# Kernel optimization log

Measured on AMD Instinct MI355X. Metric: run time of the kernel, lower is better.

## Reference

```python
import jax, jax.numpy as jnp
import numpy as np

EPS = 1e-5

def _gn(x, w, b):
    # GroupNorm with 1 group on [N, C]: normalize each row over C, then affine.
    mu = jnp.mean(x, axis=-1, keepdims=True)
    var = jnp.mean((x - mu) ** 2, axis=-1, keepdims=True)
    return (x - mu) * jax.lax.rsqrt(var + EPS) * w + b

def setup_inputs() -> dict:
    key = jax.random.key(0)
    ks = jax.random.split(key, 24)
    N_AGT, N_CTX, E, D, NC = 50000, 100000, 500000, 128, 2
    s = 0.05  # weight init scale
    inp = {
        "agts": jax.random.normal(ks[0], (N_AGT, D), jnp.float32),
        "ctx": jax.random.normal(ks[1], (N_CTX, D), jnp.float32),
        "agt_ctrs": jax.random.normal(ks[2], (N_AGT, NC), jnp.float32),
        "ctx_ctrs": jax.random.normal(ks[3], (N_CTX, NC), jnp.float32),
        "hi": jax.random.randint(ks[4], (E,), 0, N_AGT, jnp.int32),
        "wi": jax.random.randint(ks[5], (E,), 0, N_CTX, jnp.int32),
        # dist MLP: Linear(2->128, bias) + ReLU, then Linear(128->128 no bias)+GN+ReLU
        "Wd1": jax.random.normal(ks[6], (D, NC), jnp.float32) * s,
        "bd1": jnp.zeros((D,), jnp.float32),
        "Wd2": jax.random.normal(ks[7], (D, D), jnp.float32) * s,
        "gd2w": jnp.ones((D,), jnp.float32), "gd2b": jnp.zeros((D,), jnp.float32),
        # query: Linear(128->128 no bias)+GN+ReLU
        "Wq": jax.random.normal(ks[8], (D, D), jnp.float32) * s,
        "gqw": jnp.ones((D,), jnp.float32), "gqb": jnp.zeros((D,), jnp.float32),
        # ctx MLP: Linear(384->128 no bias)+GN+ReLU, then Linear(128->128 no bias)
        "Wc1": jax.random.normal(ks[9], (D, 3 * D), jnp.float32) * s,
        "gc1w": jnp.ones((D,), jnp.float32), "gc1b": jnp.zeros((D,), jnp.float32),
        "Wc2": jax.random.normal(ks[10], (D, D), jnp.float32) * s,
        # agt linear (no bias), post-scatter GN, final Linear(no bias)+GN
        "Wa": jax.random.normal(ks[11], (D, D), jnp.float32) * s,
        "gnw": jnp.ones((D,), jnp.float32), "gnb": jnp.zeros((D,), jnp.float32),
        "Wl": jax.random.normal(ks[12], (D, D), jnp.float32) * s,
        "glw": jnp.ones((D,), jnp.float32), "glb": jnp.zeros((D,), jnp.float32),
    }
    return inp

def reference(agts, ctx, agt_ctrs, ctx_ctrs, hi, wi,
              Wd1, bd1, Wd2, gd2w, gd2b, Wq, gqw, gqb,
              Wc1, gc1w, gc1b, Wc2, Wa, gnw, gnb, Wl, glw, glb):
    res = agts
    # dist branch: relative center offsets of edges -> MLP
    d = agt_ctrs[hi] - ctx_ctrs[wi]                    # [E, 2]
    d = jax.nn.relu(d @ Wd1.T + bd1)                   # [E, 128]
    d = jax.nn.relu(_gn(d @ Wd2.T, gd2w, gd2b))        # [E, 128]
    # query branch: gathered agent features
    q = jax.nn.relu(_gn(agts[hi] @ Wq.T, gqw, gqb))    # [E, 128]
    # ctx branch: concat(dist, query, gathered ctx) -> MLP
    c = jnp.concatenate([d, q, ctx[wi]], axis=1)       # [E, 384]
    c = jax.nn.relu(_gn(c @ Wc1.T, gc1w, gc1b))        # [E, 128]
    c = c @ Wc2.T                                      # [E, 128]
    # scatter-add messages back to agents
    a = agts @ Wa.T
    a = a.at[hi].add(c)
    a = jax.nn.relu(_gn(a, gnw, gnb))
    a = _gn(a @ Wl.T, glw, glb)
    return jax.nn.relu(a + res)
```

## Files before the change

### kernel.cpp

```cpp
#include <hip/hip_runtime.h>
#include <hip/hip_bf16.h>

#define D 128
#define TM 64
#define APITCH 136
#define WSLICE 16384

typedef __attribute__((ext_vector_type(8))) short short8;
typedef __attribute__((ext_vector_type(4))) float f32x4;
typedef __attribute__((ext_vector_type(2))) float f32x2;

__device__ __forceinline__ short f2bf(float f) {
    union { float f; unsigned u; } v; v.f = f;
    unsigned r = v.u + 0x7fffu + ((v.u >> 16) & 1u);
    return (short)(r >> 16);
}
__device__ __forceinline__ float bflo(unsigned v) {
    union { unsigned u; float f; } t; t.u = v << 16; return t.f;
}
__device__ __forceinline__ float bfhi(unsigned v) {
    union { unsigned u; float f; } t; t.u = v & 0xffff0000u; return t.f;
}
__device__ __forceinline__ unsigned pkbf(float a, float b) {
    return (unsigned)(unsigned short)f2bf(a) | ((unsigned)(unsigned short)f2bf(b) << 16);
}

struct TileLDS {
    short A[TM * APITCH];
    f32x2 red[TM][4];
    f32x2 mr[TM];
};

struct WPA { const float* src[8]; int pitch[8]; int coloff[8]; };

__global__ __launch_bounds__(256)
void k_wprep(WPA a, short* __restrict__ wf) {
    int slice = blockIdx.x & 7, chunk = blockIdx.x >> 3;
    int tid = threadIdx.x, lane = tid & 63;
    int slot = chunk * 4 + (tid >> 6);
    int w = slot >> 3, t = (slot >> 2) & 1, ks = slot & 3;
    int lr = lane & 15, kh = lane >> 4;
    const float* src = a.src[slice];
    int row = w * 32 + t * 16 + lr;
    int col0 = a.coloff[slice] + ks * 32 + kh * 8;
    short8 v;
#pragma unroll
    for (int j = 0; j < 8; ++j) v[j] = f2bf(src[(size_t)row * a.pitch[slice] + col0 + j]);
    *(short8*)&wf[(size_t)slice * WSLICE + ((size_t)slot * 64 + lane) * 8] = v;
}

__device__ __forceinline__ void load_wset_pre(const short* wf, int slice, int w, int lane,
                                              short8 frag[2][4]) {
    const short8* p = (const short8*)(wf + (size_t)slice * WSLICE);
#pragma unroll
    for (int t = 0; t < 2; ++t)
#pragma unroll
        for (int ks = 0; ks < 4; ++ks)
            frag[t][ks] = p[((w * 2 + t) * 4 + ks) * 64 + lane];
}

__device__ __forceinline__ void wave_gemm(const short* A, const short8 frag[2][4],
                                          int lr, int kh, f32x4 acc[4][2]) {
#pragma unroll
    for (int mt = 0; mt < 4; ++mt)
#pragma unroll
        for (int t = 0; t < 2; ++t)
            acc[mt][t] = (f32x4){0.f, 0.f, 0.f, 0.f};
#pragma unroll
    for (int ks = 0; ks < 4; ++ks) {
        short8 a[4];
#pragma unroll
        for (int mt = 0; mt < 4; ++mt)
            a[mt] = *(const short8*)&A[(mt * 16 + lr) * APITCH + ks * 32 + kh * 8];
#pragma unroll
        for (int mt = 0; mt < 4; ++mt)
#pragma unroll
            for (int t = 0; t < 2; ++t)
                acc[mt][t] = __builtin_amdgcn_mfma_f32_16x16x32_bf16(a[mt], frag[t][ks], acc[mt][t], 0, 0, 0);
    }
}

__device__ __forceinline__ void store_acc_global(float* Y, long rbase, int M,
                                                 const f32x4 acc[4][2], int lane, int w) {
    int lr = lane & 15, hh = lane >> 4;
#pragma unroll
    for (int mt = 0; mt < 4; ++mt)
#pragma unroll
        for (int t = 0; t < 2; ++t)
#pragma unroll
            for (int r = 0; r < 4; ++r) {
                int row = mt * 16 + hh * 4 + r;
                if (rbase + row < M)
                    Y[(size_t)(rbase + row) * D + w * 32 + t * 16 + lr] = acc[mt][t][r];
            }
}

__device__ __forceinline__ void store_acc_pk(unsigned* Y, long rbase, int M,
                                             const f32x4 acc[4][2], int lane, int w) {
    int lr = lane & 15, hh = lane >> 4;
#pragma unroll
    for (int mt = 0; mt < 4; ++mt)
#pragma unroll
        for (int r = 0; r < 4; ++r) {
            int row = mt * 16 + hh * 4 + r;
            if (rbase + row < M)
                Y[(size_t)(rbase + row) * 64 + w * 16 + lr] = pkbf(acc[mt][0][r], acc[mt][1][r]);
        }
}

__device__ __forceinline__ void gn_stats(TileLDS& L, const f32x4 acc[4][2],
                                         int tid, int lane, int w) {
    int lr = lane & 15, hh = lane >> 4;
#pragma unroll
    for (int mt = 0; mt < 4; ++mt)
#pragma unroll
        for (int r = 0; r < 4; ++r) {
            float s = acc[mt][0][r] + acc[mt][1][r];
            float q = acc[mt][0][r] * acc[mt][0][r] + acc[mt][1][r] * acc[mt][1][r];
            s += __shfl_xor(s, 1); q += __shfl_xor(q, 1);
            s += __shfl_xor(s, 2); q += __shfl_xor(q, 2);
            s += __shfl_xor(s, 4); q += __shfl_xor(q, 4);
            s += __shfl_xor(s, 8); q += __shfl_xor(q, 8);
            if (lr == 0) {
                int row = mt * 16 + hh * 4 + r;
                L.red[row][w] = (f32x2){s, q};
            }
        }
    __syncthreads();
    if (tid < TM) {
        f32x2 a0 = L.red[tid][0], a1 = L.red[tid][1], a2 = L.red[tid][2], a3 = L.red[tid][3];
        float s = a0[0] + a1[0] + a2[0] + a3[0];
        float q = a0[1] + a1[1] + a2[1] + a3[1];
        float mu = s * (1.f / 128.f);
        float var = q * (1.f / 128.f) - mu * mu;
        L.mr[tid] = (f32x2){mu, rsqrtf(var + 1e-5f)};
    }
    __syncthreads();
}

__device__ __forceinline__ void gn_reg(TileLDS& L, const f32x4 acc[4][2],
                                       float gw0, float gb0, float gw1, float gb1,
                                       int tid, int lane, int w) {
    gn_stats(L, acc, tid, lane, w);
    int lr = lane & 15, hh = lane >> 4, n0 = w * 32;
#pragma unroll
    for (int mt = 0; mt < 4; ++mt)
#pragma unroll
        for (int r = 0; r < 4; ++r) {
            int row = mt * 16 + hh * 4 + r;
            f32x2 m = L.mr[row];
            float v0 = (acc[mt][0][r] - m[0]) * m[1] * gw0 + gb0;
            float v1 = (acc[mt][1][r] - m[0]) * m[1] * gw1 + gb1;
            L.A[row * APITCH + n0 + lr]      = f2bf(fmaxf(v0, 0.f));
            L.A[row * APITCH + n0 + 16 + lr] = f2bf(fmaxf(v1, 0.f));
        }
    __syncthreads();
}

__device__ __forceinline__ void stage_rows_to_A(TileLDS& L, const float* X, long rbase, int M, int tid) {
#pragma unroll
    for (int it = 0; it < 8; ++it) {
        int chunk = tid + it * 256;
        int row = chunk >> 5, c4 = chunk & 31;
        long r = rbase + row;
        float4 v = (r < M) ? *(const float4*)&X[(size_t)r * D + c4 * 4] : make_float4(0.f, 0.f, 0.f, 0.f);
        short* a = &L.A[row * APITCH + c4 * 4];
        a[0] = f2bf(v.x); a[1] = f2bf(v.y); a[2] = f2bf(v.z); a[3] = f2bf(v.w);
    }
}

__global__ void k_hist(const int* __restrict__ hi, int* __restrict__ cnt, int E) {
    int i = blockIdx.x * 256 + threadIdx.x;
    if (i < E) atomicAdd(&cnt[hi[i]], 1);
}

__global__ void k_scan(const int* __restrict__ cnt, int* __restrict__ offs,
                       int* __restrict__ cursor, int n) {
    __shared__ int wsum[4];
    __shared__ int carry_s;
    int tid = threadIdx.x, lane = tid & 63, w = tid >> 6;
    if (tid == 0) carry_s = 0;
    __syncthreads();
    for (int base = 0; base < n; base += 256) {
        int i = base + tid;
        int v = (i < n) ? cnt[i] : 0;
        int x = v;
#pragma unroll
        for (int d = 1; d < 64; d <<= 1) {
            int t = __shfl_up(x, d);
            if (lane >= d) x += t;
        }
        if (lane == 63) wsum[w] = x;
        __syncthreads();
        int woff = 0;
        for (int j = 0; j < w; ++j) woff += wsum[j];
        int carry = carry_s;
        int excl = carry + woff + x - v;
        if (i < n) { offs[i] = excl; cursor[i] = excl; }
        __syncthreads();
        if (tid == 255) carry_s = carry + woff + x;
        __syncthreads();
    }
    if (tid == 0) offs[n] = carry_s;
}

__global__ void k_fill(const int* __restrict__ hi, const int* __restrict__ wi,
                       const float* __restrict__ agt_ctrs, const float* __restrict__ ctx_ctrs,
                       int* __restrict__ cursor,
                       int* __restrict__ hi_srt, int* __restrict__ wi_srt,
                       float2* __restrict__ dd_srt, int E) {
    int i = blockIdx.x * 256 + threadIdx.x;
    if (i < E) {
        int h = hi[i], c = wi[i];
        int p = atomicAdd(&cursor[h], 1);
        hi_srt[p] = h;
        wi_srt[p] = c;
        float2 dd;
        dd.x = agt_ctrs[h * 2 + 0] - ctx_ctrs[c * 2 + 0];
        dd.y = agt_ctrs[h * 2 + 1] - ctx_ctrs[c * 2 + 1];
        dd_srt[p] = dd;
    }
}

__global__ __launch_bounds__(256, 3)
void k_qpath(const float* __restrict__ agts, const short* __restrict__ wf,
             const float* __restrict__ gqw, const float* __restrict__ gqb,
             unsigned* __restrict__ qp32, float* __restrict__ abuf, int M, int ntiles) {
    __shared__ TileLDS L;
    int tid = threadIdx.x;
    int lane = tid & 63, w = tid >> 6;
    int lr = lane & 15, kh = lane >> 4;
    int n0 = w * 32;
    short8 fa[2][4], fq[2][4], fcq[2][4];
    load_wset_pre(wf, 0, w, lane, fa);
    load_wset_pre(wf, 1, w, lane, fq);
    load_wset_pre(wf, 3, w, lane, fcq);
    float gw0 = gqw[n0 + lr], gw1 = gqw[n0 + 16 + lr];
    float gb0 = gqb[n0 + lr], gb1 = gqb[n0 + 16 + lr];

    for (int tile = blockIdx.x; tile < ntiles; tile += gridDim.x) {
        long rbase = (long)tile * TM;
        stage_rows_to_A(L, agts, rbase, M, tid);
        __syncthreads();
        f32x4 acc[4][2];
        wave_gemm(L.A, fa, lr, kh, acc);
        store_acc_global(abuf, rbase, M, acc, lane, w);
        wave_gemm(L.A, fq, lr, kh, acc);
        gn_reg(L, acc, gw0, gb0, gw1, gb1, tid, lane, w);
        wave_gemm(L.A, fcq, lr, kh, acc);
        store_acc_pk(qp32, rbase, M, acc, lane, w);
        __syncthreads();
    }
}

__global__ __launch_bounds__(256, 4)
void k_ctx(const float* __restrict__ ctx, const short* __restrict__ wf,
           unsigned* __restrict__ cp32, int M, int ntiles) {
    __shared__ TileLDS L;
    int tid = threadIdx.x;
    int lane = tid & 63, w = tid >> 6;
    int lr = lane & 15, kh = lane >> 4;
    short8 fc[2][4];
    load_wset_pre(wf, 4, w, lane, fc);
    for (int tile = blockIdx.x; tile < ntiles; tile += gridDim.x) {
        long rbase = (long)tile * TM;
        stage_rows_to_A(L, ctx, rbase, M, tid);
        __syncthreads();
        f32x4 acc[4][2];
        wave_gemm(L.A, fc, lr, kh, acc);
        store_acc_pk(cp32, rbase, M, acc, lane, w);
        __syncthreads();
    }
}

__global__ __launch_bounds__(256, 3)
void k_edge(const float2* __restrict__ dd_srt,
            const int* __restrict__ hi_srt, const int* __restrict__ wi_srt,
            const float* __restrict__ Wd1, const float* __restrict__ bd1,
            const short* __restrict__ wf,
            const float* __restrict__ gd2w, const float* __restrict__ gd2b,
            const float* __restrict__ gc1w, const float* __restrict__ gc1b,
            const unsigned* __restrict__ qp32, const unsigned* __restrict__ cp32,
            unsigned* __restrict__ ebuf32, int E, int ntiles) {
    __shared__ TileLDS L;
    int tid = threadIdx.x;
    int lane = tid & 63, w = tid >> 6;
    int lr = lane & 15, kh = lane >> 4;
    int n0 = w * 32;
    short8 fd2[2][4], fc1[2][4], fc2[2][4];
    load_wset_pre(wf, 5, w, lane, fd2);
    load_wset_pre(wf, 2, w, lane, fc1);
    load_wset_pre(wf, 6, w, lane, fc2);
    float g2w0 = gd2w[n0 + lr], g2w1 = gd2w[n0 + 16 + lr];
    float g2b0 = gd2b[n0 + lr], g2b1 = gd2b[n0 + 16 + lr];
    float g1w0 = gc1w[n0 + lr], g1w1 = gc1w[n0 + 16 + lr];
    float g1b0 = gc1b[n0 + lr], g1b1 = gc1b[n0 + 16 + lr];

    for (int tile = blockIdx.x; tile < ntiles; tile += gridDim.x) {
        long ebase = (long)tile * TM;
        unsigned qv[16], cv[16];
#pragma unroll
        for (int mt = 0; mt < 4; ++mt)
#pragma unroll
            for (int r = 0; r < 4; ++r) {
                int row = mt * 16 + kh * 4 + r;
                long e = ebase + row;
                int h = (e < E) ? hi_srt[e] : 0;
                int c = (e < E) ? wi_srt[e] : 0;
                qv[mt * 4 + r] = qp32[(size_t)h * 64 + w * 16 + lr];
                cv[mt * 4 + r] = cp32[(size_t)c * 64 + w * 16 + lr];
            }
        {
            int row = tid >> 2, q4 = tid & 3;
            long e = ebase + row;
            bool valid = e < E;
            float2 dd = valid ? dd_srt[e] : make_float2(0.f, 0.f);
#pragma unroll
            for (int cb = 0; cb < 4; ++cb) {
                short8 ov;
#pragma unroll
                for (int j = 0; j < 8; ++j) {
                    int c = q4 * 32 + cb * 8 + j;
                    float v = valid ? fmaxf(Wd1[c * 2 + 0] * dd.x + Wd1[c * 2 + 1] * dd.y + bd1[c], 0.f) : 0.f;
                    ov[j] = f2bf(v);
                }
                *(short8*)&L.A[row * APITCH + q4 * 32 + cb * 8] = ov;
            }
        }
        __syncthreads();
        f32x4 acc[4][2];
        wave_gemm(L.A, fd2, lr, kh, acc);
        gn_reg(L, acc, g2w0, g2b0, g2w1, g2b1, tid, lane, w);
        wave_gemm(L.A, fc1, lr, kh, acc);
#pragma unroll
        for (int mt = 0; mt < 4; ++mt)
#pragma unroll
            for (int r = 0; r < 4; ++r) {
                unsigned vq = qv[mt * 4 + r];
                unsigned vc = cv[mt * 4 + r];
                acc[mt][0][r] += bflo(vq) + bflo(vc);
                acc[mt][1][r] += bfhi(vq) + bfhi(vc);
            }
        gn_reg(L, acc, g1w0, g1b0, g1w1, g1b1, tid, lane, w);
        wave_gemm(L.A, fc2, lr, kh, acc);
#pragma unroll
        for (int mt = 0; mt < 4; ++mt)
#pragma unroll
            for (int r = 0; r < 4; ++r) {
                int erow = mt * 16 + kh * 4 + r;
                long e = ebase + erow;
                if (e < E)
                    ebuf32[(size_t)e * 64 + w * 16 + lr] = pkbf(acc[mt][0][r], acc[mt][1][r]);
            }
        __syncthreads();
    }
}

__global__ __launch_bounds__(256, 4)
void k_final(const float* __restrict__ abuf, const float* __restrict__ agts,
             const unsigned* __restrict__ ebuf32, const int* __restrict__ offs,
             const short* __restrict__ wf,
             const float* __restrict__ gnw, const float* __restrict__ gnb,
             const float* __restrict__ glw, const float* __restrict__ glb,
             float* __restrict__ out, int M, int ntiles) {
    __shared__ TileLDS L;
    int tid = threadIdx.x;
    int lane = tid & 63, w = tid >> 6;
    int lr = lane & 15, kh = lane >> 4;
    int n0 = w * 32;
    short8 fl[2][4];
    load_wset_pre(wf, 7, w, lane, fl);
    float gw0 = glw[n0 + lr], gw1 = glw[n0 + 16 + lr];
    float gb0 = glb[n0 + lr], gb1 = glb[n0 + 16 + lr];

    for (int tile = blockIdx.x; tile < ntiles; tile += gridDim.x) {
        long rbase = (long)tile * TM;
        int row = tid >> 2, q4 = tid & 3;
        long r = rbase + row;
        float x[32];
        {
            const float4* src = (const float4*)(abuf + (size_t)r * D + q4 * 32);
#pragma unroll
            for (int i = 0; i < 8; ++i) {
                float4 v = (r < M) ? src[i] : make_float4(0.f, 0.f, 0.f, 0.f);
                x[i * 4 + 0] = v.x; x[i * 4 + 1] = v.y; x[i * 4 + 2] = v.z; x[i * 4 + 3] = v.w;
            }
            if (r < M) {
                int s0 = offs[r], e1 = offs[r + 1];
                for (int p = s0; p < e1; ++p) {
                    const unsigned* er = ebuf32 + (size_t)p * 64 + q4 * 16;
#pragma unroll
                    for (int j = 0; j < 16; ++j) {
                        unsigned v = er[j];
                        x[j]      += bflo(v);
                        x[16 + j] += bfhi(v);
                    }
                }
            }
            float s = 0.f, q = 0.f;
#pragma unroll
            for (int i = 0; i < 32; ++i) { s += x[i]; q += x[i] * x[i]; }
            L.red[row][q4] = (f32x2){s, q};
        }
        __syncthreads();
        if (tid < TM) {
            f32x2 a0 = L.red[tid][0], a1 = L.red[tid][1], a2 = L.red[tid][2], a3 = L.red[tid][3];
            float s = a0[0] + a1[0] + a2[0] + a3[0];
            float q = a0[1] + a1[1] + a2[1] + a3[1];
            float mu = s * (1.f / 128.f);
            float var = q * (1.f / 128.f) - mu * mu;
            L.mr[tid] = (f32x2){mu, rsqrtf(var + 1e-5f)};
        }
        __syncthreads();
        {
            f32x2 m = L.mr[row];
#pragma unroll
            for (int cb = 0; cb < 4; ++cb) {
                short8 ov;
#pragma unroll
                for (int j = 0; j < 8; ++j) {
                    int c = q4 * 32 + cb * 8 + j;
                    float v = (x[cb * 8 + j] - m[0]) * m[1] * gnw[c] + gnb[c];
                    ov[j] = f2bf(fmaxf(v, 0.f));
                }
                *(short8*)&L.A[row * APITCH + q4 * 32 + cb * 8] = ov;
            }
        }
        __syncthreads();
        f32x4 acc[4][2];
        wave_gemm(L.A, fl, lr, kh, acc);
        gn_stats(L, acc, tid, lane, w);
#pragma unroll
        for (int mt = 0; mt < 4; ++mt)
#pragma unroll
            for (int rr = 0; rr < 4; ++rr) {
                int orow = mt * 16 + kh * 4 + rr;
                long gr = rbase + orow;
                if (gr < M) {
                    f32x2 m = L.mr[orow];
                    float v0 = (acc[mt][0][rr] - m[0]) * m[1] * gw0 + gb0;
                    float v1 = (acc[mt][1][rr] - m[0]) * m[1] * gw1 + gb1;
                    v0 += agts[(size_t)gr * D + n0 + lr];
                    v1 += agts[(size_t)gr * D + n0 + 16 + lr];
                    out[(size_t)gr * D + n0 + lr]      = fmaxf(v0, 0.f);
                    out[(size_t)gr * D + n0 + 16 + lr] = fmaxf(v1, 0.f);
                }
            }
        __syncthreads();
    }
}

extern "C" void kernel_launch(void* const* d_in, const int* in_sizes, int n_in,
                              void* d_out, int out_size, void* d_ws, size_t ws_size,
                              hipStream_t stream) {
    const float* agts     = (const float*)d_in[0];
    const float* ctx      = (const float*)d_in[1];
    const float* agt_ctrs = (const float*)d_in[2];
    const float* ctx_ctrs = (const float*)d_in[3];
    const int*   hi       = (const int*)d_in[4];
    const int*   wi       = (const int*)d_in[5];
    const float* Wd1 = (const float*)d_in[6];
    const float* bd1 = (const float*)d_in[7];
    const float* Wd2 = (const float*)d_in[8];
    const float* gd2w = (const float*)d_in[9];
    const float* gd2b = (const float*)d_in[10];
    const float* Wq  = (const float*)d_in[11];
    const float* gqw = (const float*)d_in[12];
    const float* gqb = (const float*)d_in[13];
    const float* Wc1 = (const float*)d_in[14];
    const float* gc1w = (const float*)d_in[15];
    const float* gc1b = (const float*)d_in[16];
    const float* Wc2 = (const float*)d_in[17];
    const float* Wa  = (const float*)d_in[18];
    const float* gnw = (const float*)d_in[19];
    const float* gnb = (const float*)d_in[20];
    const float* Wl  = (const float*)d_in[21];
    const float* glw = (const float*)d_in[22];
    const float* glb = (const float*)d_in[23];

    int N_AGT = in_sizes[0] / D;
    int N_CTX = in_sizes[1] / D;
    int E     = in_sizes[4];
    float* out = (float*)d_out;

    short*    wf     = (short*)d_ws;
    unsigned* qp32   = (unsigned*)(wf + 8 * (size_t)WSLICE);
    unsigned* cp32   = qp32 + (size_t)N_AGT * 64;
    float*    abuf   = (float*)(cp32 + (size_t)N_CTX * 64);
    unsigned* ebuf32 = (unsigned*)(abuf + (size_t)N_AGT * D);
    int*      cnt    = (int*)(ebuf32 + (size_t)E * 64);
    int*      offs   = cnt + N_AGT;
    int*      cursor = offs + N_AGT + 1;
    int*      hi_srt = cursor + N_AGT;
    int*      wi_srt = hi_srt + E;
    float2*   dd_srt = (float2*)(wi_srt + E);

    int tq = (N_AGT + TM - 1) / TM;
    int tc = (N_CTX + TM - 1) / TM;
    int te = (E + TM - 1) / TM;
    int ge = (E + 255) / 256;
    int gq = tq < 768 ? tq : 768;
    int gc = tc < 1536 ? tc : 1536;
    int gE = te < 1536 ? te : 1536;
    int gf = tq < 768 ? tq : 768;

    WPA wpa;
    wpa.src[0] = Wa;  wpa.pitch[0] = 128; wpa.coloff[0] = 0;
    wpa.src[1] = Wq;  wpa.pitch[1] = 128; wpa.coloff[1] = 0;
    wpa.src[2] = Wc1; wpa.pitch[2] = 384; wpa.coloff[2] = 0;
    wpa.src[3] = Wc1; wpa.pitch[3] = 384; wpa.coloff[3] = 128;
    wpa.src[4] = Wc1; wpa.pitch[4] = 384; wpa.coloff[4] = 256;
    wpa.src[5] = Wd2; wpa.pitch[5] = 128; wpa.coloff[5] = 0;
    wpa.src[6] = Wc2; wpa.pitch[6] = 128; wpa.coloff[6] = 0;
    wpa.src[7] = Wl;  wpa.pitch[7] = 128; wpa.coloff[7] = 0;

    hipMemsetAsync(cnt, 0, (size_t)N_AGT * sizeof(int), stream);
    k_wprep<<<64, 256, 0, stream>>>(wpa, wf);
    k_hist<<<ge, 256, 0, stream>>>(hi, cnt, E);
    k_scan<<<1, 256, 0, stream>>>(cnt, offs, cursor, N_AGT);
    k_fill<<<ge, 256, 0, stream>>>(hi, wi, agt_ctrs, ctx_ctrs, cursor,
                                   hi_srt, wi_srt, dd_srt, E);

    k_qpath<<<gq, 256, 0, stream>>>(agts, wf, gqw, gqb, qp32, abuf, N_AGT, tq);
    k_ctx<<<gc, 256, 0, stream>>>(ctx, wf, cp32, N_CTX, tc);
    k_edge<<<gE, 256, 0, stream>>>(dd_srt, hi_srt, wi_srt, Wd1, bd1, wf,
                                   gd2w, gd2b, gc1w, gc1b, qp32, cp32, ebuf32, E, te);
    k_final<<<gf, 256, 0, stream>>>(abuf, agts, ebuf32, offs, wf,
                                    gnw, gnb, glw, glb, out, N_AGT, tq);
}
```

Baseline: 1.002 ms.

## Stream edge-kernel weight fragments from cache to raise occupancy

The edge kernel no longer holds three full weight sets in registers. Each GEMM now loads its weight fragments from global memory (served by L2/L1) per k-step, and the launch bound rises to 8 blocks per SM with a larger grid. The q/ctx gathers move from a register prefetch at the top of the tile to just after the second GEMM, using edge indices staged in LDS. This cuts register pressure so more waves can hide gather latency, at the cost of repeated weight loads and a gather that is no longer prefetched ahead of the GEMMs.

New measurement: 1.122 ms. 1.12x slower.

```diff
diff --git a/kernel.cpp b/kernel.cpp
--- a/kernel.cpp
+++ b/kernel.cpp
@@ -29,6 +29,8 @@
     short A[TM * APITCH];
     f32x2 red[TM][4];
     f32x2 mr[TM];
+    int hi_s[TM];
+    int wi_s[TM];
 };
 
 struct WPA { const float* src[8]; int pitch[8]; int coloff[8]; };
@@ -77,6 +79,29 @@
 #pragma unroll
             for (int t = 0; t < 2; ++t)
                 acc[mt][t] = __builtin_amdgcn_mfma_f32_16x16x32_bf16(a[mt], frag[t][ks], acc[mt][t], 0, 0, 0);
+    }
+}
+
+__device__ __forceinline__ void wave_gemm_l2(const short* A, const short8* wslice,
+                                             int w, int lane, int lr, int kh, f32x4 acc[4][2]) {
+#pragma unroll
+    for (int mt = 0; mt < 4; ++mt)
+#pragma unroll
+        for (int t = 0; t < 2; ++t)
+            acc[mt][t] = (f32x4){0.f, 0.f, 0.f, 0.f};
+#pragma unroll
+    for (int ks = 0; ks < 4; ++ks) {
+        short8 a[4];
+#pragma unroll
+        for (int mt = 0; mt < 4; ++mt)
+            a[mt] = *(const short8*)&A[(mt * 16 + lr) * APITCH + ks * 32 + kh * 8];
+#pragma unroll
+        for (int t = 0; t < 2; ++t) {
+            short8 f = wslice[((w * 2 + t) * 4 + ks) * 64 + lane];
+#pragma unroll
+            for (int mt = 0; mt < 4; ++mt)
+                acc[mt][t] = __builtin_amdgcn_mfma_f32_16x16x32_bf16(a[mt], f, acc[mt][t], 0, 0, 0);
+        }
     }
 }
 
@@ -273,7 +298,7 @@
     }
 }
 
-__global__ __launch_bounds__(256, 3)
+__global__ __launch_bounds__(256, 8)
 void k_edge(const float2* __restrict__ dd_srt,
             const int* __restrict__ hi_srt, const int* __restrict__ wi_srt,
             const float* __restrict__ Wd1, const float* __restrict__ bd1,
@@ -287,10 +312,6 @@
     int lane = tid & 63, w = tid >> 6;
     int lr = lane & 15, kh = lane >> 4;
     int n0 = w * 32;
-    short8 fd2[2][4], fc1[2][4], fc2[2][4];
-    load_wset_pre(wf, 5, w, lane, fd2);
-    load_wset_pre(wf, 2, w, lane, fc1);
-    load_wset_pre(wf, 6, w, lane, fc2);
     float g2w0 = gd2w[n0 + lr], g2w1 = gd2w[n0 + 16 + lr];
     float g2b0 = gd2b[n0 + lr], g2b1 = gd2b[n0 + 16 + lr];
     float g1w0 = gc1w[n0 + lr], g1w1 = gc1w[n0 + 16 + lr];
@@ -298,18 +319,17 @@
 
     for (int tile = blockIdx.x; tile < ntiles; tile += gridDim.x) {
         long ebase = (long)tile * TM;
-        unsigned qv[16], cv[16];
-#pragma unroll
-        for (int mt = 0; mt < 4; ++mt)
-#pragma unroll
-            for (int r = 0; r < 4; ++r) {
-                int row = mt * 16 + kh * 4 + r;
-                long e = ebase + row;
-                int h = (e < E) ? hi_srt[e] : 0;
-                int c = (e < E) ? wi_srt[e] : 0;
-                qv[mt * 4 + r] = qp32[(size_t)h * 64 + w * 16 + lr];
-                cv[mt * 4 + r] = cp32[(size_t)c * 64 + w * 16 + lr];
-            }
+        const short* wfo = wf;
+        asm volatile("" : "+s"(wfo));
+        const short8* pd2 = (const short8*)(wfo + 5 * (size_t)WSLICE);
+        const short8* pc1 = (const short8*)(wfo + 2 * (size_t)WSLICE);
+        const short8* pc2 = (const short8*)(wfo + 6 * (size_t)WSLICE);
+
+        if (tid < TM) {
+            long e = ebase + tid;
+            L.hi_s[tid] = (e < E) ? hi_srt[e] : 0;
+            L.wi_s[tid] = (e < E) ? wi_srt[e] : 0;
+        }
         {
             int row = tid >> 2, q4 = tid & 3;
             long e = ebase + row;
@@ -329,20 +349,21 @@
         }
         __syncthreads();
         f32x4 acc[4][2];
-        wave_gemm(L.A, fd2, lr, kh, acc);
+        wave_gemm_l2(L.A, pd2, w, lane, lr, kh, acc);
         gn_reg(L, acc, g2w0, g2b0, g2w1, g2b1, tid, lane, w);
-        wave_gemm(L.A, fc1, lr, kh, acc);
+        wave_gemm_l2(L.A, pc1, w, lane, lr, kh, acc);
 #pragma unroll
         for (int mt = 0; mt < 4; ++mt)
 #pragma unroll
             for (int r = 0; r < 4; ++r) {
-                unsigned vq = qv[mt * 4 + r];
-                unsigned vc = cv[mt * 4 + r];
+                int row = mt * 16 + kh * 4 + r;
+                unsigned vq = qp32[(size_t)L.hi_s[row] * 64 + w * 16 + lr];
+                unsigned vc = cp32[(size_t)L.wi_s[row] * 64 + w * 16 + lr];
                 acc[mt][0][r] += bflo(vq) + bflo(vc);
                 acc[mt][1][r] += bfhi(vq) + bfhi(vc);
             }
         gn_reg(L, acc, g1w0, g1b0, g1w1, g1b1, tid, lane, w);
-        wave_gemm(L.A, fc2, lr, kh, acc);
+        wave_gemm_l2(L.A, pc2, w, lane, lr, kh, acc);
 #pragma unroll
         for (int mt = 0; mt < 4; ++mt)
 #pragma unroll
@@ -501,7 +522,7 @@
     int ge = (E + 255) / 256;
     int gq = tq < 768 ? tq : 768;
     int gc = tc < 1536 ? tc : 1536;
-    int gE = te < 1536 ? te : 1536;
+    int gE = te < 2048 ? te : 2048;
     int gf = tq < 768 ? tq : 768;
 
     WPA wpa;
```
